# Kernel optimization log

Measured on AMD Instinct MI355X. Metric: run time of the kernel, lower is better.

Reference implementation:

```python
import jax, jax.numpy as jnp
import numpy as np

B, T, C = 4, 2048, 1024
H, D = 16, 64  # num_heads, head_size; H*D == C


def setup_inputs() -> dict:
    key = jax.random.key(0)
    k1, k2, k3 = jax.random.split(key, 3)
    x = jax.random.normal(k1, (B, T, C), dtype=jnp.float32)
    w_qkv = jax.random.normal(k2, (C, 3 * C), dtype=jnp.float32) * (C ** -0.5)
    w_out = jax.random.normal(k3, (C, C), dtype=jnp.float32) * (C ** -0.5)
    b_out = jnp.zeros((C,), dtype=jnp.float32)
    return {"x": x, "w_qkv": w_qkv, "w_out": w_out, "b_out": b_out}


def reference(x, w_qkv, w_out, b_out):
    Bb, Tt, Cc = x.shape
    qkv = x @ w_qkv                        # [B,T,3C]
    q, k, v = jnp.split(qkv, 3, axis=2)
    # [B,T,C] -> [B,H,T,D]
    q = q.reshape(Bb, Tt, H, D).transpose(0, 2, 1, 3)
    k = k.reshape(Bb, Tt, H, D).transpose(0, 2, 1, 3)
    v = v.reshape(Bb, Tt, H, D).transpose(0, 2, 1, 3)
    scores = jnp.einsum('bhqd,bhkd->bhqk', q, k) * (D ** -0.5)
    causal = jnp.tril(jnp.ones((Tt, Tt), dtype=bool))
    scores = jnp.where(causal, scores, -jnp.inf)
    attn = jax.nn.softmax(scores, axis=-1)  # dropout is identity in eval mode
    out = jnp.einsum('bhqk,bhkd->bhqd', attn, v)
    out = out.transpose(0, 2, 1, 3).reshape(Bb, Tt, Cc)
    return out @ w_out + b_out
```

## Files before the change

### kernel.cpp

```cpp
#include <hip/hip_runtime.h>

typedef __bf16 bf16;
typedef __bf16 bf16x4 __attribute__((ext_vector_type(4)));
typedef __bf16 bf16x8 __attribute__((ext_vector_type(8)));
typedef float  f32x4  __attribute__((ext_vector_type(4)));

#define MFMA16(A_, B_, C_) __builtin_amdgcn_mfma_f32_16x16x32_bf16((A_), (B_), (C_), 0, 0, 0)

#define BB 4
#define TT 2048
#define CC 1024
#define HH 16
#define DD 64
#define MM (BB * TT)
#define N_QKV (3 * CC)
#define LDSS 72
#define BSTRIDE 36
#define QSCALE2 0.18033688f

static __device__ __forceinline__ void store_lds8(bf16* p, bf16x8 v) {
  bf16x4 lo, hi;
#pragma unroll
  for (int i = 0; i < 4; i++) { lo[i] = v[i]; hi[i] = v[i + 4]; }
  *(bf16x4*)p = lo;
  *(bf16x4*)(p + 4) = hi;
}

static __device__ __forceinline__ bf16x8 load_lds8(const bf16* p) {
  bf16x4 lo = *(const bf16x4*)p;
  bf16x4 hi = *(const bf16x4*)(p + 4);
  bf16x8 v;
#pragma unroll
  for (int i = 0; i < 4; i++) { v[i] = lo[i]; v[i + 4] = hi[i]; }
  return v;
}

static __device__ __forceinline__ void async_cp16(const bf16* g, bf16* l) {
  __builtin_amdgcn_global_load_lds(
      (const __attribute__((address_space(1))) void*)g,
      (__attribute__((address_space(3))) void*)l, 16, 0, 0);
}

__global__ __launch_bounds__(256) void sniff_k(const unsigned short* __restrict__ u,
                                               int* __restrict__ flag) {
  __shared__ int s;
  if (threadIdx.x == 0) s = 0;
  __syncthreads();
  int c = 0;
  for (int i = threadIdx.x; i < 65536; i += 256)
    if ((u[i] & 0x7F80u) == 0x7F80u) c = 1;
  if (c) atomicOr(&s, 1);
  __syncthreads();
  if (threadIdx.x == 0) *flag = s;
}

__global__ __launch_bounds__(256) void cvt_k(const void* __restrict__ in,
                                             bf16* __restrict__ out,
                                             const int* __restrict__ flag,
                                             size_t off) {
  const int fl = *flag;
  const size_t i = ((size_t)blockIdx.x * 256 + threadIdx.x) * 8;
  if (fl) {
    f32x4 a = *(const f32x4*)((const float*)in + off + i);
    f32x4 b = *(const f32x4*)((const float*)in + off + i + 4);
    bf16x8 o;
#pragma unroll
    for (int j = 0; j < 4; j++) { o[j] = (bf16)a[j]; o[4 + j] = (bf16)b[j]; }
    *(bf16x8*)(out + i) = o;
  } else {
    *(bf16x8*)(out + i) = *(const bf16x8*)((const bf16*)in + off + i);
  }
}

__global__ __launch_bounds__(256) void transpose_k(const void* __restrict__ in,
                                                   bf16* __restrict__ out,
                                                   int R, int C,
                                                   const int* __restrict__ flag) {
  __shared__ bf16 tile[32][33];
  const int fl = *flag;
  const int c0 = blockIdx.x * 32, r0 = blockIdx.y * 32;
  const int tx = threadIdx.x & 31, ty = threadIdx.x >> 5;
#pragma unroll
  for (int i = ty; i < 32; i += 8) {
    const size_t idx = (size_t)(r0 + i) * C + c0 + tx;
    tile[i][tx] = fl ? (bf16)((const float*)in)[idx] : ((const bf16*)in)[idx];
  }
  __syncthreads();
#pragma unroll
  for (int i = ty; i < 32; i += 8)
    out[(size_t)(c0 + i) * R + r0 + tx] = tile[tx][i];
}

template <int EPI>
__global__ __launch_bounds__(256) void gemm_lds(const bf16* __restrict__ A,
                                                const bf16* __restrict__ Bt,
                                                const void* __restrict__ biasv,
                                                void* __restrict__ Cv,
                                                const int* __restrict__ flag,
                                                size_t aoff, size_t coff,
                                                int M, int N, int K,
                                                int lda, int ldc) {
  const int fl = *flag;
  __shared__ __align__(16) bf16 sA[128 * 32];
  __shared__ __align__(16) bf16 sB[128 * 32];
  const int tid = threadIdx.x;
  const int lane = tid & 63, wave = tid >> 6;
  const int quad = lane >> 4, l15 = lane & 15;
  const int wr = wave >> 1, wc = wave & 1;
  const int m0 = blockIdx.x * 128, n0 = blockIdx.y * 128;
  const int grow = lane >> 2;
  const int gcol = (lane & 3) * 8;

  f32x4 acc[4][4];
#pragma unroll
  for (int i = 0; i < 4; i++)
#pragma unroll
    for (int j = 0; j < 4; j++) {
      f32x4 z = {0.f, 0.f, 0.f, 0.f};
      acc[i][j] = z;
    }

  const bf16* Ag = A + aoff + (size_t)(m0 + wave * 32 + grow) * lda + gcol;
  const bf16* Bg = Bt + (size_t)(n0 + wave * 32 + grow) * K + gcol;
  bf16* sAw = sA + wave * 32 * 32;
  bf16* sBw = sB + wave * 32 * 32;

  for (int k0 = 0; k0 < K; k0 += 32) {
    __syncthreads();
    async_cp16(Ag, sAw);
    async_cp16(Ag + (size_t)16 * lda, sAw + 16 * 32);
    async_cp16(Bg, sBw);
    async_cp16(Bg + (size_t)16 * K, sBw + 16 * 32);
    Ag += 32;
    Bg += 32;
    __syncthreads();

    bf16x8 af[4], bfr[4];
#pragma unroll
    for (int mi = 0; mi < 4; mi++)
      af[mi] = *(const bf16x8*)(sA + (wr * 64 + mi * 16 + l15) * 32 + quad * 8);
#pragma unroll
    for (int ni = 0; ni < 4; ni++)
      bfr[ni] = *(const bf16x8*)(sB + (wc * 64 + ni * 16 + l15) * 32 + quad * 8);
#pragma unroll
    for (int mi = 0; mi < 4; mi++)
#pragma unroll
      for (int ni = 0; ni < 4; ni++)
        acc[mi][ni] = MFMA16(af[mi], bfr[ni], acc[mi][ni]);
  }

#pragma unroll
  for (int mi = 0; mi < 4; mi++) {
#pragma unroll
    for (int r = 0; r < 4; r++) {
      const int m = m0 + wr * 64 + mi * 16 + quad * 4 + r;
#pragma unroll
      for (int ni = 0; ni < 4; ni++) {
        const int n = n0 + wc * 64 + ni * 16 + l15;
        float v = acc[mi][ni][r];
        const size_t idx = coff + (size_t)m * ldc + n;
        if (EPI == 1) {
          v += fl ? ((const float*)biasv)[n] : (float)((const bf16*)biasv)[n];
          if (fl) ((float*)Cv)[idx] = v;
          else    ((bf16*)Cv)[idx] = (bf16)v;
        } else {
          ((bf16*)Cv)[idx] = (bf16)v;
        }
      }
    }
  }
}

template <int EPI, bool AF>
__global__ __launch_bounds__(256) void gemm_bt(const void* __restrict__ Av,
                                               const bf16* __restrict__ Bt,
                                               const void* __restrict__ biasv,
                                               void* __restrict__ Cv,
                                               const int* __restrict__ flag,
                                               size_t aoff, size_t coff,
                                               int M, int N, int K,
                                               int lda, int ldc) {
  const int fl = *flag;
  const bool af32 = AF && (fl != 0);
  __shared__ __align__(16) bf16 sA[128 * 32];
  __shared__ __align__(16) bf16 sB[128 * 32];
  const int tid = threadIdx.x;
  const int lane = tid & 63, wave = tid >> 6;
  const int quad = lane >> 4, l15 = lane & 15;
  const int wr = wave >> 1, wc = wave & 1;
  const int m0 = blockIdx.x * 128, n0 = blockIdx.y * 128;
  const int srow = tid >> 2;
  const int scol = (tid & 3) * 8;

  f32x4 acc[4][4];
#pragma unroll
  for (int i = 0; i < 4; i++)
#pragma unroll
    for (int j = 0; j < 4; j++) {
      f32x4 z = {0.f, 0.f, 0.f, 0.f};
      acc[i][j] = z;
    }

  const size_t abase0 = aoff + (size_t)(m0 + srow) * lda + scol;
  const size_t abase1 = abase0 + (size_t)64 * lda;
  const bf16* Bg0 = Bt + (size_t)(n0 + srow) * K + scol;
  const bf16* Bg1 = Bg0 + (size_t)64 * K;

  for (int k0 = 0; k0 < K; k0 += 32) {
    bf16x8 a0, a1;
    if (af32) {
      const float* Af = (const float*)Av;
      f32x4 p00 = *(const f32x4*)(Af + abase0 + k0);
      f32x4 p01 = *(const f32x4*)(Af + abase0 + k0 + 4);
      f32x4 p10 = *(const f32x4*)(Af + abase1 + k0);
      f32x4 p11 = *(const f32x4*)(Af + abase1 + k0 + 4);
#pragma unroll
      for (int i = 0; i < 4; i++) {
        a0[i] = (bf16)p00[i]; a0[i + 4] = (bf16)p01[i];
        a1[i] = (bf16)p10[i]; a1[i + 4] = (bf16)p11[i];
      }
    } else {
      const bf16* Ab = (const bf16*)Av;
      a0 = *(const bf16x8*)(Ab + abase0 + k0);
      a1 = *(const bf16x8*)(Ab + abase1 + k0);
    }
    bf16x8 b0 = *(const bf16x8*)(Bg0 + k0);
    bf16x8 b1 = *(const bf16x8*)(Bg1 + k0);
    __syncthreads();
    *(bf16x8*)(sA + srow * 32 + scol) = a0;
    *(bf16x8*)(sA + (64 + srow) * 32 + scol) = a1;
    *(bf16x8*)(sB + srow * 32 + scol) = b0;
    *(bf16x8*)(sB + (64 + srow) * 32 + scol) = b1;
    __syncthreads();

    bf16x8 af[4], bfr[4];
#pragma unroll
    for (int mi = 0; mi < 4; mi++)
      af[mi] = *(const bf16x8*)(sA + (wr * 64 + mi * 16 + l15) * 32 + quad * 8);
#pragma unroll
    for (int ni = 0; ni < 4; ni++)
      bfr[ni] = *(const bf16x8*)(sB + (wc * 64 + ni * 16 + l15) * 32 + quad * 8);
#pragma unroll
    for (int mi = 0; mi < 4; mi++)
#pragma unroll
      for (int ni = 0; ni < 4; ni++)
        acc[mi][ni] = MFMA16(af[mi], bfr[ni], acc[mi][ni]);
  }

#pragma unroll
  for (int mi = 0; mi < 4; mi++) {
#pragma unroll
    for (int r = 0; r < 4; r++) {
      const int m = m0 + wr * 64 + mi * 16 + quad * 4 + r;
#pragma unroll
      for (int ni = 0; ni < 4; ni++) {
        const int n = n0 + wc * 64 + ni * 16 + l15;
        float v = acc[mi][ni][r];
        const size_t idx = coff + (size_t)m * ldc + n;
        if (EPI == 1) {
          v += fl ? ((const float*)biasv)[n] : (float)((const bf16*)biasv)[n];
          if (fl) ((float*)Cv)[idx] = v;
          else    ((bf16*)Cv)[idx] = (bf16)v;
        } else {
          ((bf16*)Cv)[idx] = (bf16)v;
        }
      }
    }
  }
}

template <int EPI, bool AF, bool WF>
__global__ __launch_bounds__(256) void gemm_nt(const void* __restrict__ Av,
                                               const void* __restrict__ Wv,
                                               const void* __restrict__ biasv,
                                               void* __restrict__ Cv,
                                               const int* __restrict__ flag,
                                               size_t aoff, size_t coff,
                                               int M, int N, int K,
                                               int lda, int ldc) {
  const int fl = *flag;
  const bool af32 = AF && (fl != 0);
  const bool wf32 = WF && (fl != 0);
  __shared__ __align__(16) bf16 sA[128 * 32];
  __shared__ __align__(16) bf16 sB[128 * BSTRIDE];
  const int tid = threadIdx.x;
  const int lane = tid & 63, wave = tid >> 6;
  const int quad = lane >> 4, l15 = lane & 15;
  const int wr = wave >> 1, wc = wave & 1;
  const int m0 = blockIdx.x * 128, n0 = blockIdx.y * 128;
  const int arow = tid >> 2, acol = (tid & 3) * 8;
  const int wk = tid >> 3, wn = (tid & 7) * 16;

  f32x4 acc[4][4];
#pragma unroll
  for (int i = 0; i < 4; i++)
#pragma unroll
    for (int j = 0; j < 4; j++) {
      f32x4 z = {0.f, 0.f, 0.f, 0.f};
      acc[i][j] = z;
    }

  const size_t abase0 = aoff + (size_t)(m0 + arow) * lda + acol;
  const size_t abase1 = abase0 + (size_t)64 * lda;

  for (int k0 = 0; k0 < K; k0 += 32) {
    bf16x8 a0, a1;
    if (af32) {
      const float* Af = (const float*)Av;
      f32x4 p00 = *(const f32x4*)(Af + abase0 + k0);
      f32x4 p01 = *(const f32x4*)(Af + abase0 + k0 + 4);
      f32x4 p10 = *(const f32x4*)(Af + abase1 + k0);
      f32x4 p11 = *(const f32x4*)(Af + abase1 + k0 + 4);
#pragma unroll
      for (int i = 0; i < 4; i++) {
        a0[i] = (bf16)p00[i]; a0[i + 4] = (bf16)p01[i];
        a1[i] = (bf16)p10[i]; a1[i + 4] = (bf16)p11[i];
      }
    } else {
      const bf16* Ab = (const bf16*)Av;
      a0 = *(const bf16x8*)(Ab + abase0 + k0);
      a1 = *(const bf16x8*)(Ab + abase1 + k0);
    }
    bf16 wreg[16];
    const size_t wbase = (size_t)(k0 + wk) * N + n0 + wn;
    if (wf32) {
      const float* Wf = (const float*)Wv;
      f32x4 q0 = *(const f32x4*)(Wf + wbase);
      f32x4 q1 = *(const f32x4*)(Wf + wbase + 4);
      f32x4 q2 = *(const f32x4*)(Wf + wbase + 8);
      f32x4 q3 = *(const f32x4*)(Wf + wbase + 12);
#pragma unroll
      for (int i = 0; i < 4; i++) {
        wreg[i] = (bf16)q0[i];      wreg[4 + i] = (bf16)q1[i];
        wreg[8 + i] = (bf16)q2[i];  wreg[12 + i] = (bf16)q3[i];
      }
    } else {
      const bf16* Wb = (const bf16*)Wv;
      bf16x8 w0 = *(const bf16x8*)(Wb + wbase);
      bf16x8 w1 = *(const bf16x8*)(Wb + wbase + 8);
#pragma unroll
      for (int i = 0; i < 8; i++) { wreg[i] = w0[i]; wreg[8 + i] = w1[i]; }
    }
    __syncthreads();
    *(bf16x8*)(sA + arow * 32 + acol) = a0;
    *(bf16x8*)(sA + (64 + arow) * 32 + acol) = a1;
#pragma unroll
    for (int i = 0; i < 16; i++)
      sB[(wn + i) * BSTRIDE + wk] = wreg[i];
    __syncthreads();

    bf16x8 af[4], bfr[4];
#pragma unroll
    for (int mi = 0; mi < 4; mi++)
      af[mi] = *(const bf16x8*)(sA + (wr * 64 + mi * 16 + l15) * 32 + quad * 8);
#pragma unroll
    for (int ni = 0; ni < 4; ni++)
      bfr[ni] = load_lds8(sB + (wc * 64 + ni * 16 + l15) * BSTRIDE + quad * 8);
#pragma unroll
    for (int mi = 0; mi < 4; mi++)
#pragma unroll
      for (int ni = 0; ni < 4; ni++)
        acc[mi][ni] = MFMA16(af[mi], bfr[ni], acc[mi][ni]);
  }

#pragma unroll
  for (int mi = 0; mi < 4; mi++) {
#pragma unroll
    for (int r = 0; r < 4; r++) {
      const int m = m0 + wr * 64 + mi * 16 + quad * 4 + r;
#pragma unroll
      for (int ni = 0; ni < 4; ni++) {
        const int n = n0 + wc * 64 + ni * 16 + l15;
        float v = acc[mi][ni][r];
        const size_t idx = coff + (size_t)m * ldc + n;
        if (EPI == 1) {
          v += fl ? ((const float*)biasv)[n] : (float)((const bf16*)biasv)[n];
          if (fl) ((float*)Cv)[idx] = v;
          else    ((bf16*)Cv)[idx] = (bf16)v;
        } else {
          ((bf16*)Cv)[idx] = (bf16)v;
        }
      }
    }
  }
}

__global__ __launch_bounds__(256) void attn_k(bf16* __restrict__ qkv) {
  __shared__ __align__(16) bf16 sQ[128 * LDSS];
  __shared__ __align__(16) bf16 sK[64 * LDSS];
  __shared__ __align__(16) bf16 sVt[64 * LDSS];

  const int tid = threadIdx.x;
  const int lane = tid & 63, wave = tid >> 6;
  const int quad = lane >> 4, l15 = lane & 15;
  const int bh = blockIdx.x;
  bf16* base = qkv + (size_t)(bh >> 4) * TT * N_QKV + (bh & 15) * DD;
  const bf16* Qp = base;
  const bf16* Kp = base + CC;
  const bf16* Vp = base + 2 * CC;

  const int krow = tid >> 2;
  const int kcol = (tid & 3) * 16;
  const int vkey = tid & 31;
  const int vcol = (tid >> 5) * 8;

  bf16x8 ones;
  {
    const bf16 o = (l15 == 0) ? (bf16)1.0f : (bf16)0.0f;
#pragma unroll
    for (int i = 0; i < 8; i++) ones[i] = o;
  }

  const int qt = 15 - (int)blockIdx.y;
  const int q0 = qt * 128;

#pragma unroll
  for (int p = 0; p < 2; p++) {
    const int r = p * 64 + krow;
    const bf16* src = Qp + (size_t)(q0 + r) * N_QKV + kcol;
    bf16x8 v0 = *(const bf16x8*)src;
    bf16x8 v1 = *(const bf16x8*)(src + 8);
#pragma unroll
    for (int i = 0; i < 8; i++) {
      v0[i] = (bf16)((float)v0[i] * QSCALE2);
      v1[i] = (bf16)((float)v1[i] * QSCALE2);
    }
    *(bf16x8*)(sQ + r * LDSS + kcol) = v0;
    *(bf16x8*)(sQ + r * LDSS + kcol + 8) = v1;
  }

  bf16x8 kr0, kr1, vr0, vr1;
  {
    const bf16* kp = Kp + (size_t)krow * N_QKV + kcol;
    kr0 = *(const bf16x8*)kp;
    kr1 = *(const bf16x8*)(kp + 8);
    vr0 = *(const bf16x8*)(Vp + (size_t)vkey * N_QKV + vcol);
    vr1 = *(const bf16x8*)(Vp + (size_t)(32 + vkey) * N_QKV + vcol);
  }
  __syncthreads();

  bf16x8 aq[2][2];
#pragma unroll
  for (int mi = 0; mi < 2; mi++) {
    const bf16* qp = sQ + (size_t)(wave * 32 + mi * 16 + l15) * LDSS + quad * 8;
    aq[mi][0] = *(const bf16x8*)qp;
    aq[mi][1] = *(const bf16x8*)(qp + 32);
  }

  f32x4 Oacc[2][4];
  f32x4 lacc[2];
#pragma unroll
  for (int mi = 0; mi < 2; mi++) {
    f32x4 z = {0.f, 0.f, 0.f, 0.f};
    lacc[mi] = z;
#pragma unroll
    for (int nt = 0; nt < 4; nt++) Oacc[mi][nt] = z;
  }

  const int jmax = q0 + 64;
  const int wave_row0 = q0 + wave * 32;
  bf16* sP = sQ + (size_t)(wave * 32) * LDSS;

  for (int j0 = 0; j0 <= jmax; j0 += 64) {
    __syncthreads();
    *(bf16x8*)(sK + krow * LDSS + kcol) = kr0;
    *(bf16x8*)(sK + krow * LDSS + kcol + 8) = kr1;
#pragma unroll
    for (int i = 0; i < 8; i++) {
      sVt[(vcol + i) * LDSS + vkey] = vr0[i];
      sVt[(vcol + i) * LDSS + 32 + vkey] = vr1[i];
    }
    __syncthreads();

    if (j0 + 64 <= jmax) {
      const bf16* kp = Kp + (size_t)(j0 + 64 + krow) * N_QKV + kcol;
      kr0 = *(const bf16x8*)kp;
      kr1 = *(const bf16x8*)(kp + 8);
      vr0 = *(const bf16x8*)(Vp + (size_t)(j0 + 64 + vkey) * N_QKV + vcol);
      vr1 = *(const bf16x8*)(Vp + (size_t)(j0 + 96 + vkey) * N_QKV + vcol);
    }

    if (j0 <= wave_row0 + 31) {
      f32x4 S[2][4];
#pragma unroll
      for (int nt = 0; nt < 4; nt++) {
        const bf16* kp = sK + (size_t)(nt * 16 + l15) * LDSS + quad * 8;
        bf16x8 bk0 = *(const bf16x8*)kp;
        bf16x8 bk1 = *(const bf16x8*)(kp + 32);
#pragma unroll
        for (int mi = 0; mi < 2; mi++) {
          f32x4 acc = {0.f, 0.f, 0.f, 0.f};
          acc = MFMA16(aq[mi][0], bk0, acc);
          acc = MFMA16(aq[mi][1], bk1, acc);
          S[mi][nt] = acc;
        }
      }

      const bool needmask = (j0 + 63 > wave_row0);
#pragma unroll
      for (int mi = 0; mi < 2; mi++)
#pragma unroll
        for (int nt = 0; nt < 4; nt++) {
          const int kc = j0 + nt * 16 + l15;
#pragma unroll
          for (int r = 0; r < 4; r++) {
            float e = __builtin_amdgcn_exp2f(S[mi][nt][r]);
            if (needmask && kc > wave_row0 + mi * 16 + quad * 4 + r) e = 0.f;
            sP[(size_t)(mi * 16 + quad * 4 + r) * LDSS + nt * 16 + l15] =
                (bf16)e;
          }
        }

      bf16x8 ap[2][2];
#pragma unroll
      for (int mi = 0; mi < 2; mi++) {
        const bf16* pp = sP + (size_t)(mi * 16 + l15) * LDSS + quad * 8;
        ap[mi][0] = *(const bf16x8*)pp;
        ap[mi][1] = *(const bf16x8*)(pp + 32);
        lacc[mi] = MFMA16(ap[mi][0], ones, lacc[mi]);
        lacc[mi] = MFMA16(ap[mi][1], ones, lacc[mi]);
      }
#pragma unroll
      for (int nt = 0; nt < 4; nt++) {
        const bf16* vp = sVt + (size_t)(nt * 16 + l15) * LDSS + quad * 8;
        bf16x8 bv0 = *(const bf16x8*)vp;
        bf16x8 bv1 = *(const bf16x8*)(vp + 32);
#pragma unroll
        for (int mi = 0; mi < 2; mi++) {
          Oacc[mi][nt] = MFMA16(ap[mi][0], bv0, Oacc[mi][nt]);
          Oacc[mi][nt] = MFMA16(ap[mi][1], bv1, Oacc[mi][nt]);
        }
      }
    }
  }

#pragma unroll
  for (int mi = 0; mi < 2; mi++)
#pragma unroll
    for (int r = 0; r < 4; r++) {
      const float lv = __shfl(lacc[mi][r], lane & 48, 64);
      const float invl = 1.0f / lv;
      const int t = q0 + wave * 32 + mi * 16 + quad * 4 + r;
#pragma unroll
      for (int nt = 0; nt < 4; nt++)
        base[(size_t)t * N_QKV + nt * 16 + l15] =
            (bf16)(Oacc[mi][nt][r] * invl);
    }
}

extern "C" void kernel_launch(void* const* d_in, const int* in_sizes, int n_in,
                              void* d_out, int out_size, void* d_ws, size_t ws_size,
                              hipStream_t stream) {
  const void* x = d_in[0];
  const void* w_qkv = d_in[1];
  const void* w_out = d_in[2];
  const void* b_out = d_in[3];

  int* flag = (int*)d_ws;
  char* p = (char*)d_ws + 256;
  bf16* wqkvT = (bf16*)p;
  bf16* woutT = wqkvT + (size_t)N_QKV * CC;

  const size_t wT_bytes = ((size_t)N_QKV * CC + (size_t)CC * CC) * 2;
  const size_t qkv_bytes = (size_t)MM * N_QKV * 2;
  const size_t need_A = 256 + wT_bytes + qkv_bytes;
  const size_t need_B = 256 + wT_bytes + (size_t)TT * N_QKV * 2;

  sniff_k<<<1, 256, 0, stream>>>((const unsigned short*)x, flag);

  if (ws_size >= need_A) {
    bf16* qkv = woutT + (size_t)CC * CC;
    bf16* xb = qkv + (size_t)MM * N_QKV;
    const size_t slack = ws_size - need_A;

    transpose_k<<<dim3(N_QKV / 32, CC / 32), 256, 0, stream>>>(w_qkv, wqkvT, CC, N_QKV, flag);
    transpose_k<<<dim3(CC / 32, CC / 32), 256, 0, stream>>>(w_out, woutT, CC, CC, flag);

    const size_t full_xb = (size_t)MM * CC * 2;
    const size_t half_xb = full_xb / 2;
    if (slack >= full_xb) {
      cvt_k<<<(MM * CC) / 2048, 256, 0, stream>>>(x, xb, flag, 0);
      gemm_lds<0><<<dim3(MM / 128, N_QKV / 128), 256, 0, stream>>>(
          xb, wqkvT, nullptr, qkv, flag, 0, 0, MM, N_QKV, CC, CC, N_QKV);
    } else if (slack >= half_xb) {
      for (int m0 = 0; m0 < MM; m0 += 4096) {
        cvt_k<<<(4096 * CC) / 2048, 256, 0, stream>>>(x, xb, flag, (size_t)m0 * CC);
        gemm_lds<0><<<dim3(4096 / 128, N_QKV / 128), 256, 0, stream>>>(
            xb, wqkvT, nullptr, qkv, flag, 0, (size_t)m0 * N_QKV,
            4096, N_QKV, CC, CC, N_QKV);
      }
    } else {
      gemm_bt<0, true><<<dim3(MM / 128, N_QKV / 128), 256, 0, stream>>>(
          x, wqkvT, nullptr, qkv, flag, 0, 0, MM, N_QKV, CC, CC, N_QKV);
    }

    attn_k<<<dim3(BB * HH, 16), 256, 0, stream>>>(qkv);

    gemm_lds<1><<<dim3(MM / 128, CC / 128), 256, 0, stream>>>(
        qkv, woutT, b_out, d_out, flag, 0, 0, MM, CC, CC, N_QKV, CC);
  } else if (ws_size >= need_B) {
    bf16* qkv = woutT + (size_t)CC * CC;
    transpose_k<<<dim3(N_QKV / 32, CC / 32), 256, 0, stream>>>(w_qkv, wqkvT, CC, N_QKV, flag);
    transpose_k<<<dim3(CC / 32, CC / 32), 256, 0, stream>>>(w_out, woutT, CC, CC, flag);
    for (int b = 0; b < BB; b++) {
      const size_t xoff = (size_t)b * TT * CC;
      gemm_bt<0, true><<<dim3(TT / 128, N_QKV / 128), 256, 0, stream>>>(
          x, wqkvT, nullptr, qkv, flag, xoff, 0, TT, N_QKV, CC, CC, N_QKV);
      attn_k<<<dim3(HH, 16), 256, 0, stream>>>(qkv);
      gemm_lds<1><<<dim3(TT / 128, CC / 128), 256, 0, stream>>>(
          qkv, woutT, b_out, d_out, flag, 0, xoff, TT, CC, CC, N_QKV, CC);
    }
  } else {
    bf16* qkvb = (bf16*)p;
    for (int b = 0; b < BB; b++) {
      const size_t xoff = (size_t)b * TT * CC;
      gemm_nt<0, true, true><<<dim3(TT / 128, N_QKV / 128), 256, 0, stream>>>(
          x, w_qkv, nullptr, qkvb, flag, xoff, 0, TT, N_QKV, CC, CC, N_QKV);
      attn_k<<<dim3(HH, 16), 256, 0, stream>>>(qkvb);
      gemm_nt<1, false, true><<<dim3(TT / 128, CC / 128), 256, 0, stream>>>(
          qkvb, w_out, b_out, d_out, flag, 0, xoff, TT, CC, CC, N_QKV, CC);
    }
  }
}
```

Before: 305.9 us.

## Rewrite causal attention to read K and pre-transposed V directly, skipping LDS staging

```diff
diff --git a/kernel.cpp b/kernel.cpp
--- a/kernel.cpp
+++ b/kernel.cpp
@@ -89,6 +89,23 @@
 #pragma unroll
   for (int i = ty; i < 32; i += 8)
     out[(size_t)(c0 + i) * R + r0 + tx] = tile[tx][i];
+}
+
+__global__ __launch_bounds__(256) void vtrans_k(const bf16* __restrict__ qkv,
+                                                bf16* __restrict__ vt) {
+  __shared__ bf16 tile[32][33];
+  const int bh = blockIdx.z;
+  const int t0 = blockIdx.x * 32, d0 = blockIdx.y * 32;
+  const bf16* src = qkv + (size_t)(bh >> 4) * TT * N_QKV + 2 * CC + (bh & 15) * DD;
+  const int tx = threadIdx.x & 31, ty = threadIdx.x >> 5;
+#pragma unroll
+  for (int i = ty; i < 32; i += 8)
+    tile[i][tx] = src[(size_t)(t0 + i) * N_QKV + d0 + tx];
+  __syncthreads();
+  bf16* dst = vt + ((size_t)bh * DD + d0) * TT + t0;
+#pragma unroll
+  for (int i = ty; i < 32; i += 8)
+    dst[(size_t)i * TT + tx] = tile[tx][i];
 }
 
 template <int EPI>
@@ -385,7 +402,136 @@
   }
 }
 
-__global__ __launch_bounds__(256) void attn_k(bf16* __restrict__ qkv) {
+__global__ __launch_bounds__(256) void attn_k(bf16* __restrict__ qkv,
+                                              const bf16* __restrict__ vt) {
+  __shared__ __align__(16) bf16 sP[128 * LDSS];
+
+  const int tid = threadIdx.x;
+  const int lane = tid & 63, wave = tid >> 6;
+  const int quad = lane >> 4, l15 = lane & 15;
+  const int bh = blockIdx.x;
+  bf16* base = qkv + (size_t)(bh >> 4) * TT * N_QKV + (bh & 15) * DD;
+  const bf16* Qp = base;
+  const bf16* Kp = base + CC;
+  const bf16* vhead = vt + (size_t)bh * DD * TT;
+
+  const int qt = 15 - (int)blockIdx.y;
+  const int q0 = qt * 128;
+  const int wave_row0 = q0 + wave * 32;
+  bf16* sPw = sP + (size_t)(wave * 32) * LDSS;
+
+  bf16x8 ones;
+  {
+    const bf16 o = (l15 == 0) ? (bf16)1.0f : (bf16)0.0f;
+#pragma unroll
+    for (int i = 0; i < 8; i++) ones[i] = o;
+  }
+
+  bf16x8 aq[2][2];
+#pragma unroll
+  for (int mi = 0; mi < 2; mi++)
+#pragma unroll
+    for (int ks = 0; ks < 2; ks++) {
+      bf16x8 v = *(const bf16x8*)(Qp + (size_t)(wave_row0 + mi * 16 + l15) * N_QKV +
+                                  ks * 32 + quad * 8);
+#pragma unroll
+      for (int i = 0; i < 8; i++) v[i] = (bf16)((float)v[i] * QSCALE2);
+      aq[mi][ks] = v;
+    }
+
+  f32x4 Oacc[2][4];
+  f32x4 lacc[2];
+#pragma unroll
+  for (int mi = 0; mi < 2; mi++) {
+    f32x4 z = {0.f, 0.f, 0.f, 0.f};
+    lacc[mi] = z;
+#pragma unroll
+    for (int nt = 0; nt < 4; nt++) Oacc[mi][nt] = z;
+  }
+
+  const int jend = wave_row0 + 31;
+
+  for (int j0 = 0; j0 <= jend; j0 += 64) {
+    f32x4 S[2][4];
+#pragma unroll
+    for (int mi = 0; mi < 2; mi++)
+#pragma unroll
+      for (int kt = 0; kt < 4; kt++) {
+        f32x4 z = {0.f, 0.f, 0.f, 0.f};
+        S[mi][kt] = z;
+      }
+    __builtin_amdgcn_s_setprio(1);
+#pragma unroll
+    for (int kt = 0; kt < 4; kt++) {
+      const bf16* kp = Kp + (size_t)(j0 + kt * 16 + l15) * N_QKV + quad * 8;
+      bf16x8 k0 = *(const bf16x8*)kp;
+      bf16x8 k1 = *(const bf16x8*)(kp + 32);
+      S[0][kt] = MFMA16(k0, aq[0][0], S[0][kt]);
+      S[0][kt] = MFMA16(k1, aq[0][1], S[0][kt]);
+      S[1][kt] = MFMA16(k0, aq[1][0], S[1][kt]);
+      S[1][kt] = MFMA16(k1, aq[1][1], S[1][kt]);
+    }
+    __builtin_amdgcn_s_setprio(0);
+
+    const bool needmask = (j0 + 63 > wave_row0);
+#pragma unroll
+    for (int mi = 0; mi < 2; mi++) {
+      const int qg = wave_row0 + mi * 16 + l15;
+#pragma unroll
+      for (int kt = 0; kt < 4; kt++) {
+        const int kb = j0 + kt * 16 + quad * 4;
+        bf16x4 pk;
+#pragma unroll
+        for (int r = 0; r < 4; r++) {
+          float e = __builtin_amdgcn_exp2f(S[mi][kt][r]);
+          if (needmask && (kb + r > qg)) e = 0.f;
+          pk[r] = (bf16)e;
+        }
+        *(bf16x4*)(sPw + (size_t)(mi * 16 + l15) * LDSS + kt * 16 + quad * 4) = pk;
+      }
+    }
+
+    bf16x8 ap0[2], ap1[2];
+#pragma unroll
+    for (int mi = 0; mi < 2; mi++) {
+      const bf16* pp = sPw + (size_t)(mi * 16 + l15) * LDSS + quad * 8;
+      ap0[mi] = *(const bf16x8*)pp;
+      ap1[mi] = *(const bf16x8*)(pp + 32);
+    }
+    __builtin_amdgcn_s_setprio(1);
+#pragma unroll
+    for (int mi = 0; mi < 2; mi++) {
+      lacc[mi] = MFMA16(ap0[mi], ones, lacc[mi]);
+      lacc[mi] = MFMA16(ap1[mi], ones, lacc[mi]);
+    }
+#pragma unroll
+    for (int nt = 0; nt < 4; nt++) {
+      const bf16* vp = vhead + (size_t)(nt * 16 + l15) * TT + j0 + quad * 8;
+      bf16x8 v0 = *(const bf16x8*)vp;
+      bf16x8 v1 = *(const bf16x8*)(vp + 32);
+      Oacc[0][nt] = MFMA16(ap0[0], v0, Oacc[0][nt]);
+      Oacc[0][nt] = MFMA16(ap1[0], v1, Oacc[0][nt]);
+      Oacc[1][nt] = MFMA16(ap0[1], v0, Oacc[1][nt]);
+      Oacc[1][nt] = MFMA16(ap1[1], v1, Oacc[1][nt]);
+    }
+    __builtin_amdgcn_s_setprio(0);
+  }
+
+#pragma unroll
+  for (int mi = 0; mi < 2; mi++)
+#pragma unroll
+    for (int r = 0; r < 4; r++) {
+      const float lv = __shfl(lacc[mi][r], lane & 48, 64);
+      const float invl = 1.0f / lv;
+      const int t = q0 + wave * 32 + mi * 16 + quad * 4 + r;
+#pragma unroll
+      for (int nt = 0; nt < 4; nt++)
+        base[(size_t)t * N_QKV + nt * 16 + l15] =
+            (bf16)(Oacc[mi][nt][r] * invl);
+    }
+}
+
+__global__ __launch_bounds__(256) void attn_s(bf16* __restrict__ qkv) {
   __shared__ __align__(16) bf16 sQ[128 * LDSS];
   __shared__ __align__(16) bf16 sK[64 * LDSS];
   __shared__ __align__(16) bf16 sVt[64 * LDSS];
@@ -582,6 +728,9 @@
       cvt_k<<<(MM * CC) / 2048, 256, 0, stream>>>(x, xb, flag, 0);
       gemm_lds<0><<<dim3(MM / 128, N_QKV / 128), 256, 0, stream>>>(
           xb, wqkvT, nullptr, qkv, flag, 0, 0, MM, N_QKV, CC, CC, N_QKV);
+      bf16* vt = xb;
+      vtrans_k<<<dim3(TT / 32, DD / 32, BB * HH), 256, 0, stream>>>(qkv, vt);
+      attn_k<<<dim3(BB * HH, 16), 256, 0, stream>>>(qkv, vt);
     } else if (slack >= half_xb) {
       for (int m0 = 0; m0 < MM; m0 += 4096) {
         cvt_k<<<(4096 * CC) / 2048, 256, 0, stream>>>(x, xb, flag, (size_t)m0 * CC);
@@ -589,12 +738,12 @@
             xb, wqkvT, nullptr, qkv, flag, 0, (size_t)m0 * N_QKV,
             4096, N_QKV, CC, CC, N_QKV);
       }
+      attn_s<<<dim3(BB * HH, 16), 256, 0, stream>>>(qkv);
     } else {
       gemm_bt<0, true><<<dim3(MM / 128, N_QKV / 128), 256, 0, stream>>>(
           x, wqkvT, nullptr, qkv, flag, 0, 0, MM, N_QKV, CC, CC, N_QKV);
-    }
-
-    attn_k<<<dim3(BB * HH, 16), 256, 0, stream>>>(qkv);
+      attn_s<<<dim3(BB * HH, 16), 256, 0, stream>>>(qkv);
+    }
 
     gemm_lds<1><<<dim3(MM / 128, CC / 128), 256, 0, stream>>>(
         qkv, woutT, b_out, d_out, flag, 0, 0, MM, CC, CC, N_QKV, CC);
@@ -606,7 +755,7 @@
       const size_t xoff = (size_t)b * TT * CC;
       gemm_bt<0, true><<<dim3(TT / 128, N_QKV / 128), 256, 0, stream>>>(
           x, wqkvT, nullptr, qkv, flag, xoff, 0, TT, N_QKV, CC, CC, N_QKV);
-      attn_k<<<dim3(HH, 16), 256, 0, stream>>>(qkv);
+      attn_s<<<dim3(HH, 16), 256, 0, stream>>>(qkv);
       gemm_lds<1><<<dim3(TT / 128, CC / 128), 256, 0, stream>>>(
           qkv, woutT, b_out, d_out, flag, 0, xoff, TT, CC, CC, N_QKV, CC);
     }
@@ -616,7 +765,7 @@
       const size_t xoff = (size_t)b * TT * CC;
       gemm_nt<0, true, true><<<dim3(TT / 128, N_QKV / 128), 256, 0, stream>>>(
           x, w_qkv, nullptr, qkvb, flag, xoff, 0, TT, N_QKV, CC, CC, N_QKV);
-      attn_k<<<dim3(HH, 16), 256, 0, stream>>>(qkvb);
+      attn_s<<<dim3(HH, 16), 256, 0, stream>>>(qkvb);
       gemm_nt<1, false, true><<<dim3(TT / 128, CC / 128), 256, 0, stream>>>(
           qkvb, w_out, b_out, d_out, flag, 0, xoff, TT, CC, CC, N_QKV, CC);
     }
```

Result: slower. 383.3 us (+25.3%).
